# Kernel optimization log

Measured on AMD Instinct MI355X. Metric: run time of the kernel, lower is better.

Reference implementation:

```python
import math
import jax, jax.numpy as jnp
import numpy as np

# irreps: 128x0e + 64x1o + 32x2e  -> (mul, l, parity)
IRREPS = [(128, 0, 1), (64, 1, -1), (32, 2, 1)]
IR_SET = {(l, p) for _, l, p in IRREPS}
FEAT_DIM = sum(m * (2 * l + 1) for m, l, _ in IRREPS)   # 480
N_NODES = 32768
TOTAL_MUL = sum(m for m, _, _ in IRREPS)                # 224


def _su2_cg(j1, j2, j3, m1, m2, m3):
    if m1 + m2 != m3:
        return 0.0
    f = math.factorial
    pref = math.sqrt((2 * j3 + 1) * f(j3 + j1 - j2) * f(j3 - j1 + j2) * f(j1 + j2 - j3) / f(j1 + j2 + j3 + 1))
    pref *= math.sqrt(f(j3 + m3) * f(j3 - m3) * f(j1 - m1) * f(j1 + m1) * f(j2 - m2) * f(j2 + m2))
    s = 0.0
    vmin = max(0, j2 - j3 - m1, j1 - j3 + m2)
    vmax = min(j2 + m2, j1 - m1, j1 + j2 - j3)
    for v in range(vmin, vmax + 1):
        s += (-1.0) ** v / (f(v) * f(j1 + j2 - j3 - v) * f(j1 - m1 - v) * f(j2 + m2 - v) * f(j3 - j2 + m1 + v) * f(j3 - j1 - m2 + v))
    return pref * s


def _q(l):
    # change of basis real <- complex spherical harmonics (e3nn convention)
    q = np.zeros((2 * l + 1, 2 * l + 1), dtype=complex)
    for m in range(-l, 0):
        q[l + m, l + abs(m)] = 1 / np.sqrt(2)
        q[l + m, l - abs(m)] = -1j / np.sqrt(2)
    q[l, l] = 1.0
    for m in range(1, l + 1):
        q[l + m, l + abs(m)] = (-1) ** m / np.sqrt(2)
        q[l + m, l - abs(m)] = 1j * (-1) ** m / np.sqrt(2)
    return (-1j) ** l * q


def _wigner3j(l1, l2, l3):
    Cc = np.zeros((2 * l1 + 1, 2 * l2 + 1, 2 * l3 + 1))
    for m1 in range(-l1, l1 + 1):
        for m2 in range(-l2, l2 + 1):
            m3 = m1 + m2
            if -l3 <= m3 <= l3:
                Cc[l1 + m1, l2 + m2, l3 + m3] = _su2_cg(l1, l2, l3, m1, m2, m3)
    C = np.einsum('ai,bj,ck,abc->ijk', _q(l1), _q(l2), np.conj(_q(l3)), Cc.astype(complex))
    Cr, Ci = np.real(C), np.imag(C)
    C = Cr if np.linalg.norm(Cr) >= np.linalg.norm(Ci) else Ci
    return (C / np.linalg.norm(C)).astype(np.float32)


# CG-coupling paths ('uvu' connection, shared internal weights of shape [mul1, mul2])
PATHS = []
_off = 0
for _i1, (_m1, _l1, _p1) in enumerate(IRREPS):
    for _i2, (_m2, _l2, _p2) in enumerate(IRREPS):
        for _l3 in range(abs(_l1 - _l2), _l1 + _l2 + 1):
            _p3 = _p1 * _p2
            if (_l3, _p3) in IR_SET:
                PATHS.append((_i1, _i2, _l3, _p3, _off, _m1 * _m2))
                _off += _m1 * _m2
TPW_SIZE = _off  # 55296
W3J = {(IRREPS[i1][1], IRREPS[i2][1], l3): None for i1, i2, l3, _, _, _ in PATHS}
for (_l1, _l2, _l3) in list(W3J.keys()):
    W3J[(_l1, _l2, _l3)] = jnp.asarray(_wigner3j(_l1, _l2, _l3))
COUPLED_MUL = {}
for _i1, _i2, _l3, _p3, _, _ in PATHS:
    COUPLED_MUL[(_l3, _p3)] = COUPLED_MUL.get((_l3, _p3), 0) + IRREPS[_i1][0]


def _split(feat):
    blocks, o = [], 0
    for mul, l, _ in IRREPS:
        d = mul * (2 * l + 1)
        blocks.append(feat[:, o:o + d].reshape(feat.shape[0], mul, 2 * l + 1))
        o += d
    return blocks


def _merge(blocks):
    return jnp.concatenate([x.reshape(x.shape[0], -1) for x in blocks], axis=-1)


def _lin(blocks, ws):
    # e3nn o3.Linear between identical simplified irreps: per-l channel mixing, 1/sqrt(fan_in)
    return [jnp.einsum('nui,uv->nvi', x, w) / np.sqrt(x.shape[1]) for x, w in zip(blocks, ws)]


def _normgate(blocks, w1, b1, w2, b2):
    # invariants: raw scalars for l=0, channel norms for l>0
    invs = []
    for (mul, l, _), x in zip(IRREPS, blocks):
        invs.append(x[:, :, 0] if l == 0 else jnp.sqrt(jnp.sum(x * x, -1) + 1e-12))
    v = jnp.concatenate(invs, -1)                          # [N, TOTAL_MUL]
    vn = (v - v.mean(-1, keepdims=True)) / jnp.sqrt(v.var(-1, keepdims=True) + 1e-5)  # 'node' norm
    g = jax.nn.silu(jax.nn.silu(vn @ w1 + b1) @ w2 + b2)   # 2-layer MLP gate
    out, o = [], 0
    for (mul, l, _), x in zip(IRREPS, blocks):
        out.append(x * g[:, o:o + mul, None])
        o += mul
    return out


def _cg_couple(b1, b2, tp_w):
    grouped = {(0, 1): [], (1, -1): [], (2, 1): []}
    for i1, i2, l3, p3, off, size in PATHS:
        m1, l1, _ = IRREPS[i1]
        m2, l2, _ = IRREPS[i2]
        w = tp_w[off:off + size].reshape(m1, m2)
        t = jnp.einsum('nvj,uv->nuj', b2[i2], w) / np.sqrt(m2)   # mix v-channels into u (small intermediate)
        y = jnp.einsum('nui,nuj,ijk->nuk', b1[i1], t, W3J[(l1, l2, l3)])
        grouped[(l3, p3)].append(y)
    return {k: jnp.concatenate(v, axis=1) for k, v in grouped.items()}


def _forward(feat, pre_w0, pre_w1, pre_w2, pre_ng_w1, pre_ng_b1, pre_ng_w2, pre_ng_b2,
             tp_w, post_w0, post_w1, post_w2, post_ng_w1, post_ng_b1, post_ng_w2, post_ng_b2):
    blocks = _split(feat)
    pre = _normgate(_lin(blocks, (pre_w0, pre_w1, pre_w2)), pre_ng_w1, pre_ng_b1, pre_ng_w2, pre_ng_b2)
    coupled = _cg_couple(blocks, pre, tp_w)
    post_blocks = []
    for (mul, l, p), w in zip(IRREPS, (post_w0, post_w1, post_w2)):
        x = coupled[(l, p)]
        post_blocks.append(jnp.einsum('nui,uv->nvi', x, w) / np.sqrt(x.shape[1]))
    post = _normgate(post_blocks, post_ng_w1, post_ng_b1, post_ng_w2, post_ng_b2)
    # feat_dropout p=0.0 -> identity
    return feat + _merge(pre) + _merge(post)


def setup_inputs() -> dict:
    key = jax.random.key(0)
    ks = jax.random.split(key, 16)
    def n(k, shape):
        return jax.random.normal(k, shape, dtype=jnp.float32)
    return {
        'feat': n(ks[0], (N_NODES, FEAT_DIM)),
        'pre_w0': n(ks[1], (128, 128)),
        'pre_w1': n(ks[2], (64, 64)),
        'pre_w2': n(ks[3], (32, 32)),
        'pre_ng_w1': n(ks[4], (TOTAL_MUL, TOTAL_MUL)) / np.sqrt(TOTAL_MUL),
        'pre_ng_b1': jnp.zeros((TOTAL_MUL,), jnp.float32),
        'pre_ng_w2': n(ks[5], (TOTAL_MUL, TOTAL_MUL)) / np.sqrt(TOTAL_MUL),
        'pre_ng_b2': jnp.zeros((TOTAL_MUL,), jnp.float32),
        'tp_w': n(ks[6], (TPW_SIZE,)),
        'post_w0': n(ks[7], (COUPLED_MUL[(0, 1)], 128)),
        'post_w1': n(ks[8], (COUPLED_MUL[(1, -1)], 64)),
        'post_w2': n(ks[9], (COUPLED_MUL[(2, 1)], 32)),
        'post_ng_w1': n(ks[10], (TOTAL_MUL, TOTAL_MUL)) / np.sqrt(TOTAL_MUL),
        'post_ng_b1': jnp.zeros((TOTAL_MUL,), jnp.float32),
        'post_ng_w2': n(ks[11], (TOTAL_MUL, TOTAL_MUL)) / np.sqrt(TOTAL_MUL),
        'post_ng_b2': jnp.zeros((TOTAL_MUL,), jnp.float32),
    }


def reference(feat, pre_w0, pre_w1, pre_w2, pre_ng_w1, pre_ng_b1, pre_ng_w2, pre_ng_b2,
              tp_w, post_w0, post_w1, post_w2, post_ng_w1, post_ng_b1, post_ng_w2, post_ng_b2):
    return _forward(feat, pre_w0, pre_w1, pre_w2, pre_ng_w1, pre_ng_b1, pre_ng_w2, pre_ng_b2,
                    tp_w, post_w0, post_w1, post_w2, post_ng_w1, post_ng_b1, post_ng_w2, post_ng_b2)
```

## Files before the change

### kernel.cpp

```cpp
#include <hip/hip_runtime.h>
#include <cmath>
#include <complex>
#include <algorithm>

#define N_NODES  32768
#define FEAT_DIM 480
#define TMUL     224
#define NB       4
#define ST       3328

#define F0O 0
#define F1O 128
#define F2O 320
#define P0O 480
#define P1O 608
#define P2O 800
#define C0O 960
#define C1O 1184
#define C2O 2048
#define Q0O 960
#define Q1O 1088
#define Q2O 1280
#define INVO 1440
#define HO   1664
#define GO   1888

#define FSTR 240

typedef float f32x4 __attribute__((ext_vector_type(4)));
typedef short short8 __attribute__((ext_vector_type(8)));

__device__ __forceinline__ float siluf(float x){ return x * (1.0f/(1.0f + __expf(-x))); }
__device__ __forceinline__ f32x4 silu4(f32x4 x){
  f32x4 r; r.x=siluf(x.x); r.y=siluf(x.y); r.z=siluf(x.z); r.w=siluf(x.w); return r;
}
__device__ __forceinline__ f32x4 sqrt4(f32x4 x){
  f32x4 r; r.x=sqrtf(x.x); r.y=sqrtf(x.y); r.z=sqrtf(x.z); r.w=sqrtf(x.w); return r;
}

__device__ __forceinline__ float bfh(ushort h){ return __uint_as_float(((uint)h)<<16); }
__device__ __forceinline__ ushort f2bf(float f){
  uint u=__float_as_uint(f); return (ushort)((u + 0x7fffu + ((u>>16)&1u))>>16);
}
__device__ __forceinline__ f32x4 X0q(uint4 q){
  f32x4 r = {__uint_as_float(q.x<<16), __uint_as_float(q.x&0xffff0000u),
             __uint_as_float(q.y<<16), __uint_as_float(q.y&0xffff0000u)};
  return r;
}
__device__ __forceinline__ f32x4 X1q(uint4 q){
  f32x4 r = {__uint_as_float(q.z<<16), __uint_as_float(q.z&0xffff0000u),
             __uint_as_float(q.w<<16), __uint_as_float(q.w&0xffff0000u)};
  return r;
}
__device__ __forceinline__ f32x4 ldE(const uint* __restrict__ Lb, int e){
  uint2 q = *(const uint2*)&Lb[e*2];
  f32x4 r = {__uint_as_float(q.x<<16), __uint_as_float(q.x&0xffff0000u),
             __uint_as_float(q.y<<16), __uint_as_float(q.y&0xffff0000u)};
  return r;
}
__device__ __forceinline__ void stE(uint* __restrict__ Lb, int e, f32x4 x){
  uint2 q = { (uint)f2bf(x.x) | ((uint)f2bf(x.y)<<16),
              (uint)f2bf(x.z) | ((uint)f2bf(x.w)<<16) };
  *(uint2*)&Lb[e*2] = q;
}

struct W3Pack { float v[363]; };

static double factd(int n){ double f=1.0; for(int i=2;i<=n;++i) f*=(double)i; return f; }

static double su2_cg(int j1,int j2,int j3,int m1,int m2,int m3){
  if (m1+m2 != m3) return 0.0;
  double pref = std::sqrt((2.0*j3+1.0)*factd(j3+j1-j2)*factd(j3-j1+j2)*factd(j1+j2-j3)/factd(j1+j2+j3+1));
  pref *= std::sqrt(factd(j3+m3)*factd(j3-m3)*factd(j1-m1)*factd(j1+m1)*factd(j2-m2)*factd(j2+m2));
  double s=0.0;
  int vmin = std::max(0, std::max(j2-j3-m1, j1-j3+m2));
  int vmax = std::min(j2+m2, std::min(j1-m1, j1+j2-j3));
  for (int v=vmin; v<=vmax; ++v){
    double d = factd(v)*factd(j1+j2-j3-v)*factd(j1-m1-v)*factd(j2+m2-v)*factd(j3-j2+m1+v)*factd(j3-j1-m2+v);
    s += ((v&1)? -1.0 : 1.0)/d;
  }
  return pref*s;
}

typedef std::complex<double> cd;

static void qmat(int l, cd* q){
  int d=2*l+1;
  for (int a=0;a<d*d;++a) q[a]=cd(0,0);
  double is2 = 1.0/std::sqrt(2.0);
  for (int m=-l; m<0; ++m){
    int am=-m;
    q[(l+m)*d + (l+am)] = cd(is2,0);
    q[(l+m)*d + (l-am)] = cd(0,-is2);
  }
  q[l*d+l] = cd(1,0);
  for (int m=1;m<=l;++m){
    double sg = (m&1)? -1.0:1.0;
    q[(l+m)*d + (l+m)] = cd(sg*is2,0);
    q[(l+m)*d + (l-m)] = cd(0,sg*is2);
  }
  cd f = (l==0)? cd(1,0) : (l==1? cd(0,-1) : cd(-1,0));
  for (int a=0;a<d*d;++a) q[a]*=f;
}

static void wigner3j(int l1,int l2,int l3, float* out){
  int d1=2*l1+1,d2=2*l2+1,d3=2*l3+1;
  double Cc[5][5][5] = {};
  for (int m1=-l1;m1<=l1;++m1) for (int m2=-l2;m2<=l2;++m2){
    int m3=m1+m2;
    if (m3>=-l3 && m3<=l3) Cc[l1+m1][l2+m2][l3+m3] = su2_cg(l1,l2,l3,m1,m2,m3);
  }
  cd q1[25],q2[25],q3[25];
  qmat(l1,q1); qmat(l2,q2); qmat(l3,q3);
  double re[125], im[125];
  double nr=0, ni=0;
  for (int i=0;i<d1;++i) for (int j=0;j<d2;++j) for (int k=0;k<d3;++k){
    cd s(0,0);
    for (int a=0;a<d1;++a) for (int b=0;b<d2;++b) for (int c=0;c<d3;++c){
      double cc = Cc[a][b][c];
      if (cc != 0.0) s += q1[a*d1+i]*q2[b*d2+j]*std::conj(q3[c*d3+k])*cc;
    }
    int o=(i*d2+j)*d3+k;
    re[o]=s.real(); im[o]=s.imag();
    nr += s.real()*s.real(); ni += s.imag()*s.imag();
  }
  bool useRe = std::sqrt(nr) >= std::sqrt(ni);
  double nrm = std::sqrt(useRe? nr : ni);
  for (int o=0;o<d1*d2*d3;++o) out[o] = (float)((useRe? re[o] : im[o]) / nrm);
}

static W3Pack build_w3(){
  W3Pack W;
  wigner3j(0,0,0, W.v+0);
  wigner3j(0,1,1, W.v+1);
  wigner3j(0,2,2, W.v+10);
  wigner3j(1,0,1, W.v+35);
  wigner3j(1,1,0, W.v+44);
  wigner3j(1,1,2, W.v+53);
  wigner3j(1,2,1, W.v+98);
  wigner3j(2,0,2, W.v+143);
  wigner3j(2,1,1, W.v+168);
  wigner3j(2,2,0, W.v+213);
  wigner3j(2,2,2, W.v+238);
  return W;
}

__global__ __launch_bounds__(256) void prep_tpw(const float* __restrict__ tpw, float* __restrict__ wt)
{
  const int t = blockIdx.x*256 + threadIdx.x;
  if (t >= 55296) return;
  float v;
  if (t < 28672) {
    const int vv = t / 224, r = t - vv*224;
    int off, u;
    if (r < 128)      { off = 0;     u = r; }
    else if (r < 192) { off = 28672; u = r-128; }
    else              { off = 47104; u = r-192; }
    v = tpw[off + u*128 + vv] * 0.08838834764831845f;
  } else if (t < 47104) {
    const int t2 = t-28672; const int vv = t2/288, r = t2 - vv*288;
    int off, u;
    if (r < 128)      { off = 16384; u = r; }
    else if (r < 192) { off = 36864; u = r-128; }
    else if (r < 256) { off = 40960; u = r-192; }
    else              { off = 51200; u = r-256; }
    v = tpw[off + u*64 + vv] * 0.125f;
  } else {
    const int t3 = t-47104; const int vv = t3/256, r = t3 & 255;
    int off, u;
    if (r < 128)      { off = 24576; u = r; }
    else if (r < 192) { off = 45056; u = r-128; }
    else if (r < 224) { off = 53248; u = r-192; }
    else              { off = 54272; u = r-224; }
    v = tpw[off + u*32 + vv] * 0.17677669529663687f;
  }
  wt[t] = v;
}

__global__ __launch_bounds__(256) void prep_mlp(
  const float* __restrict__ pgw1, const float* __restrict__ pgw2,
  const float* __restrict__ qgw1, const float* __restrict__ qgw2,
  ushort* __restrict__ wb)
{
  const int t = blockIdx.x*256 + threadIdx.x;
  if (t >= 4*50176) return;
  const int mat = t / 50176, s = t - mat*50176;
  const float* src = (mat==0)? pgw1 : (mat==1)? pgw2 : (mat==2)? qgw1 : qgw2;
  const int e = s & 7, l = (s>>3) & 63, q = s >> 9;
  const int ct = q % 14, kt = q / 14;
  const int k = kt*32 + (l>>4)*8 + e;
  const int c = ct*16 + (l&15);
  wb[t] = f2bf(src[k*224 + c]);
}

template<int N>
__device__ __forceinline__ f32x4 matcolB(const float* __restrict__ Wg, const int wstride, const int col,
                                         const uint* __restrict__ Lb, const int inbase)
{
  f32x4 a0={}, a1={}, a2={}, a3={};
  const float* wp = Wg + col;
  #pragma unroll 2
  for (int u=0; u<N; u+=4) {
    const float wA = wp[(u+0)*wstride];
    const float wB = wp[(u+1)*wstride];
    const float wC = wp[(u+2)*wstride];
    const float wD = wp[(u+3)*wstride];
    const uint4 qa = *(const uint4*)&Lb[(inbase+u)*2];
    const uint4 qb = *(const uint4*)&Lb[(inbase+u+2)*2];
    a0 += X0q(qa)*wA;
    a1 += X1q(qa)*wB;
    a2 += X0q(qb)*wC;
    a3 += X1q(qb)*wD;
  }
  return (a0+a1)+(a2+a3);
}

template<int NJ, int M2, int JS>
__device__ __forceinline__ void tstageB(const float* __restrict__ wcol, const int wstride,
                                        const uint* __restrict__ Lb, const int pbase,
                                        f32x4 (&t)[NJ])
{
  f32x4 a0[NJ], a1[NJ];
  #pragma unroll
  for (int j=0;j<NJ;++j){ a0[j]=(f32x4){}; a1[j]=(f32x4){}; }
  #pragma unroll 2
  for (int v=0; v<M2; v+=2) {
    const float wA = wcol[v*wstride];
    const float wB = wcol[(v+1)*wstride];
    #pragma unroll
    for (int j=0;j<NJ;++j) {
      const uint4 q = *(const uint4*)&Lb[(pbase + j*JS + v)*2];
      a0[j] += X0q(q)*wA;
      a1[j] += X1q(q)*wB;
    }
  }
  #pragma unroll
  for (int j=0;j<NJ;++j) t[j] = a0[j]+a1[j];
}

__device__ __forceinline__ void normgateB(uint* __restrict__ Lb, ushort* __restrict__ Lb16,
                                          ushort* __restrict__ FT16, f32x4* __restrict__ sRed, const int c,
                                          const int B0, const int B1, const int B2,
                                          const ushort* __restrict__ wb1, const float* __restrict__ gb1,
                                          const ushort* __restrict__ wb2, const float* __restrict__ gb2)
{
  if (c < 128) {
    const uint2 q = *(const uint2*)&Lb[(B0+c)*2];
    *(uint2*)&Lb[(INVO+c)*2] = q;
  } else if (c < 192) {
    const int v = c-128;
    f32x4 s = {1e-12f,1e-12f,1e-12f,1e-12f};
    #pragma unroll
    for (int i=0;i<3;++i){ const f32x4 x = ldE(Lb, B1+i*64+v); s += x*x; }
    stE(Lb, INVO+c, sqrt4(s));
  } else if (c < 224) {
    const int v = c-192;
    f32x4 s = {1e-12f,1e-12f,1e-12f,1e-12f};
    #pragma unroll
    for (int i=0;i<5;++i){ const f32x4 x = ldE(Lb, B2+i*32+v); s += x*x; }
    stE(Lb, INVO+c, sqrt4(s));
  }
  __syncthreads();
  {
    const int w = c>>6, l = c&63;
    float s=0.f, s2=0.f, x;
    x = bfh(Lb16[(INVO+l)*4+w]);      s+=x; s2+=x*x;
    x = bfh(Lb16[(INVO+64+l)*4+w]);   s+=x; s2+=x*x;
    x = bfh(Lb16[(INVO+128+l)*4+w]);  s+=x; s2+=x*x;
    if (l < 32) { x = bfh(Lb16[(INVO+192+l)*4+w]); s+=x; s2+=x*x; }
    #pragma unroll
    for (int off=32; off>=1; off>>=1) {
      s  += __shfl_xor(s,  off, 64);
      s2 += __shfl_xor(s2, off, 64);
    }
    if (l==0) {
      const float m = s*(1.f/224.f);
      ((float*)&sRed[0])[w] = m;
      ((float*)&sRed[1])[w] = rsqrtf(s2*(1.f/224.f) - m*m + 1e-5f);
    }
  }
  __syncthreads();
  if (c < TMUL) {
    const f32x4 x = ldE(Lb, INVO+c);
    const f32x4 vn = (x - sRed[0])*sRed[1];
    FT16[0*FSTR+c]=f2bf(vn.x); FT16[1*FSTR+c]=f2bf(vn.y);
    FT16[2*FSTR+c]=f2bf(vn.z); FT16[3*FSTR+c]=f2bf(vn.w);
  }
  __syncthreads();

  const int wv = c>>6, ln = c&63;
  f32x4 m0={}, m1={}, m2={}, m3={};
  #pragma unroll
  for (int kt=0; kt<7; ++kt) {
    const short8 A = *(const short8*)&FT16[(ln&15)*FSTR + kt*32 + (ln>>4)*8];
    { const short8 B = *(const short8*)&wb1[((kt*14 + wv    )*64 + ln)*8];
      m0 = __builtin_amdgcn_mfma_f32_16x16x32_bf16(A, B, m0, 0, 0, 0); }
    { const short8 B = *(const short8*)&wb1[((kt*14 + wv + 4)*64 + ln)*8];
      m1 = __builtin_amdgcn_mfma_f32_16x16x32_bf16(A, B, m1, 0, 0, 0); }
    { const short8 B = *(const short8*)&wb1[((kt*14 + wv + 8)*64 + ln)*8];
      m2 = __builtin_amdgcn_mfma_f32_16x16x32_bf16(A, B, m2, 0, 0, 0); }
    if (wv < 2) {
      const short8 B = *(const short8*)&wb1[((kt*14 + wv +12)*64 + ln)*8];
      m3 = __builtin_amdgcn_mfma_f32_16x16x32_bf16(A, B, m3, 0, 0, 0);
    }
  }
  __syncthreads();
  if (ln < 16) {
    { const int ch=(wv   )*16+ln; const f32x4 h=silu4(m0+gb1[ch]);
      FT16[0*FSTR+ch]=f2bf(h.x); FT16[1*FSTR+ch]=f2bf(h.y); FT16[2*FSTR+ch]=f2bf(h.z); FT16[3*FSTR+ch]=f2bf(h.w); }
    { const int ch=(wv+4 )*16+ln; const f32x4 h=silu4(m1+gb1[ch]);
      FT16[0*FSTR+ch]=f2bf(h.x); FT16[1*FSTR+ch]=f2bf(h.y); FT16[2*FSTR+ch]=f2bf(h.z); FT16[3*FSTR+ch]=f2bf(h.w); }
    { const int ch=(wv+8 )*16+ln; const f32x4 h=silu4(m2+gb1[ch]);
      FT16[0*FSTR+ch]=f2bf(h.x); FT16[1*FSTR+ch]=f2bf(h.y); FT16[2*FSTR+ch]=f2bf(h.z); FT16[3*FSTR+ch]=f2bf(h.w); }
    if (wv < 2) {
      const int ch=(wv+12)*16+ln; const f32x4 h=silu4(m3+gb1[ch]);
      FT16[0*FSTR+ch]=f2bf(h.x); FT16[1*FSTR+ch]=f2bf(h.y); FT16[2*FSTR+ch]=f2bf(h.z); FT16[3*FSTR+ch]=f2bf(h.w); }
  }
  __syncthreads();
  f32x4 g0={}, g1={}, g2={}, g3={};
  #pragma unroll
  for (int kt=0; kt<7; ++kt) {
    const short8 A = *(const short8*)&FT16[(ln&15)*FSTR + kt*32 + (ln>>4)*8];
    { const short8 B = *(const short8*)&wb2[((kt*14 + wv    )*64 + ln)*8];
      g0 = __builtin_amdgcn_mfma_f32_16x16x32_bf16(A, B, g0, 0, 0, 0); }
    { const short8 B = *(const short8*)&wb2[((kt*14 + wv + 4)*64 + ln)*8];
      g1 = __builtin_amdgcn_mfma_f32_16x16x32_bf16(A, B, g1, 0, 0, 0); }
    { const short8 B = *(const short8*)&wb2[((kt*14 + wv + 8)*64 + ln)*8];
      g2 = __builtin_amdgcn_mfma_f32_16x16x32_bf16(A, B, g2, 0, 0, 0); }
    if (wv < 2) {
      const short8 B = *(const short8*)&wb2[((kt*14 + wv +12)*64 + ln)*8];
      g3 = __builtin_amdgcn_mfma_f32_16x16x32_bf16(A, B, g3, 0, 0, 0);
    }
  }
  if (ln < 16) {
    { const int ch=(wv   )*16+ln; stE(Lb, GO+ch, silu4(g0+gb2[ch])); }
    { const int ch=(wv+4 )*16+ln; stE(Lb, GO+ch, silu4(g1+gb2[ch])); }
    { const int ch=(wv+8 )*16+ln; stE(Lb, GO+ch, silu4(g2+gb2[ch])); }
    if (wv < 2) { const int ch=(wv+12)*16+ln; stE(Lb, GO+ch, silu4(g3+gb2[ch])); }
  }
  __syncthreads();
}

__device__ __forceinline__ void cg_rowB(const int r, const float* __restrict__ wt,
                                        const W3Pack& W, uint* __restrict__ Lb)
{
  f32x4 tb[3];
  tstageB<3,64,64>(wt + 28672 + r, 288, Lb, P1O, tb);
  if (r < 128) {
    const f32x4 f = ldE(Lb, F0O+r);
    #pragma unroll
    for (int k=0;k<3;++k) {
      f32x4 s = tb[0]*W.v[1+0*3+k] + tb[1]*W.v[1+1*3+k] + tb[2]*W.v[1+2*3+k];
      stE(Lb, C1O+k*288+r, f*s);
    }
  } else if (r < 192) {
    const int u=r-128;
    f32x4 y = {};
    #pragma unroll
    for (int i=0;i<3;++i) {
      f32x4 s = tb[0]*W.v[44+i*3+0] + tb[1]*W.v[44+i*3+1] + tb[2]*W.v[44+i*3+2];
      y += ldE(Lb, F1O+i*64+u)*s;
    }
    stE(Lb, C0O+128+u, y);
  } else if (r < 256) {
    const int u=r-192;
    f32x4 f[3];
    #pragma unroll
    for (int i=0;i<3;++i) f[i]=ldE(Lb, F1O+i*64+u);
    #pragma unroll
    for (int k=0;k<5;++k) {
      f32x4 y = {};
      #pragma unroll
      for (int i=0;i<3;++i) {
        f32x4 s = tb[0]*W.v[53+(i*3+0)*5+k] + tb[1]*W.v[53+(i*3+1)*5+k] + tb[2]*W.v[53+(i*3+2)*5+k];
        y += f[i]*s;
      }
      stE(Lb, C2O+k*256+128+u, y);
    }
  } else {
    const int u=r-256;
    f32x4 f[5];
    #pragma unroll
    for (int i=0;i<5;++i) f[i]=ldE(Lb, F2O+i*32+u);
    #pragma unroll
    for (int k=0;k<3;++k) {
      f32x4 y = {};
      #pragma unroll
      for (int i=0;i<5;++i) {
        f32x4 s = tb[0]*W.v[168+(i*3+0)*3+k] + tb[1]*W.v[168+(i*3+1)*3+k] + tb[2]*W.v[168+(i*3+2)*3+k];
        y += f[i]*s;
      }
      stE(Lb, C1O+k*288+256+u, y);
    }
  }
}

__device__ __forceinline__ void cg_rowC(const int r, const float* __restrict__ wt,
                                        const W3Pack& W, uint* __restrict__ Lb)
{
  f32x4 tc[5];
  tstageB<5,32,32>(wt + 47104 + r, 256, Lb, P2O, tc);
  if (r < 128) {
    const f32x4 f = ldE(Lb, F0O+r);
    #pragma unroll
    for (int k=0;k<5;++k) {
      f32x4 s = {};
      #pragma unroll
      for (int j=0;j<5;++j) s += tc[j]*W.v[10+j*5+k];
      stE(Lb, C2O+k*256+r, f*s);
    }
  } else if (r < 192) {
    const int u=r-128;
    f32x4 f[3];
    #pragma unroll
    for (int i=0;i<3;++i) f[i]=ldE(Lb, F1O+i*64+u);
    #pragma unroll
    for (int k=0;k<3;++k) {
      f32x4 y = {};
      #pragma unroll
      for (int i=0;i<3;++i) {
        f32x4 s = {};
        #pragma unroll
        for (int j=0;j<5;++j) s += tc[j]*W.v[98+(i*5+j)*3+k];
        y += f[i]*s;
      }
      stE(Lb, C1O+k*288+192+u, y);
    }
  } else if (r < 224) {
    const int u=r-192;
    f32x4 y = {};
    #pragma unroll
    for (int i=0;i<5;++i) {
      f32x4 s = {};
      #pragma unroll
      for (int j=0;j<5;++j) s += tc[j]*W.v[213+i*5+j];
      y += ldE(Lb, F2O+i*32+u)*s;
    }
    stE(Lb, C0O+192+u, y);
  } else {
    const int u=r-224;
    f32x4 f[5];
    #pragma unroll
    for (int i=0;i<5;++i) f[i]=ldE(Lb, F2O+i*32+u);
    #pragma unroll
    for (int k=0;k<5;++k) {
      f32x4 y = {};
      #pragma unroll
      for (int i=0;i<5;++i) {
        f32x4 s = {};
        #pragma unroll
        for (int j=0;j<5;++j) s += tc[j]*W.v[238+(i*5+j)*5+k];
        y += f[i]*s;
      }
      stE(Lb, C2O+k*256+224+u, y);
    }
  }
}

__global__ __launch_bounds__(256, 4) void fused4(
  const float* __restrict__ feat,
  const float* __restrict__ w0, const float* __restrict__ w1, const float* __restrict__ w2,
  const float* __restrict__ pgb1, const float* __restrict__ pgb2,
  const float* __restrict__ wt, const ushort* __restrict__ wb,
  const float* __restrict__ pw0, const float* __restrict__ pw1, const float* __restrict__ pw2,
  const float* __restrict__ qgb1, const float* __restrict__ qgb2,
  float* __restrict__ outp, const W3Pack W)
{
  __shared__ uint LbU[ST*2];
  __shared__ ushort FT16[16*FSTR];
  __shared__ f32x4 sRed[2];
  uint* Lb = LbU;
  ushort* Lb16 = (ushort*)LbU;
  const int c = threadIdx.x;
  const size_t gbase = (size_t)blockIdx.x * (FEAT_DIM*NB);

  {
    uint* FTz = (uint*)FT16;
    #pragma unroll
    for (int t=c; t<16*FSTR/2; t+=256) FTz[t] = 0;
  }

  for (int t=c; t<FEAT_DIM*NB; t+=256) {
    const float val = feat[gbase + t];
    const int nb = t / FEAT_DIM;
    const int ch = t - nb*FEAT_DIM;
    int loc;
    if (ch < 128) loc = F0O + ch;
    else if (ch < 320) { const int q = ch-128; const int u = q/3; loc = F1O + (q-u*3)*64 + u; }
    else               { const int q = ch-320; const int u = q/5; loc = F2O + (q-u*5)*32 + u; }
    Lb16[loc*4 + nb] = f2bf(val);
  }
  __syncthreads();

  {
    f32x4 a1, a2 = {};
    int o1, o2=-1; float s1, s2s=0.f;
    if (c < 128) { a1 = matcolB<128>(w0, 128, c, Lb, F0O); o1 = P0O+c; s1 = 0.08838834764831845f; }
    else { const int q=c-128; const int i=q>>6, v=q&63;
           a1 = matcolB<64>(w1, 64, v, Lb, F1O+i*64); o1 = P1O+i*64+v; s1 = 0.125f; }
    if (c < 64) { a2 = matcolB<64>(w1, 64, c, Lb, F1O+128); o2 = P1O+128+c; s2s = 0.125f; }
    else if (c < 224) { const int q=c-64; const int i=q>>5, v=q&31;
           a2 = matcolB<32>(w2, 32, v, Lb, F2O+i*32); o2 = P2O+i*32+v; s2s = 0.17677669529663687f; }
    stE(Lb, o1, a1*s1);
    if (o2 >= 0) stE(Lb, o2, a2*s2s);
  }
  __syncthreads();

  normgateB(Lb, Lb16, FT16, sRed, c, P0O, P1O, P2O, wb, pgb1, wb+50176, pgb2);
  if (c < 128) {
    stE(Lb, P0O+c, ldE(Lb,P0O+c)*ldE(Lb,GO+c));
  } else if (c < 192) {
    const int v=c-128; const f32x4 g=ldE(Lb,GO+c);
    #pragma unroll
    for (int i=0;i<3;++i) stE(Lb, P1O+i*64+v, ldE(Lb,P1O+i*64+v)*g);
  } else if (c < 224) {
    const int v=c-192; const f32x4 g=ldE(Lb,GO+c);
    #pragma unroll
    for (int i=0;i<5;++i) stE(Lb, P2O+i*32+v, ldE(Lb,P2O+i*32+v)*g);
  }
  __syncthreads();

  if (c < 224) {
    const f32x4 tA = matcolB<128>(wt, 224, c, Lb, P0O);
    if (c < 128) {
      stE(Lb, C0O+c, ldE(Lb,F0O+c)*tA*W.v[0]);
    } else if (c < 192) {
      const int u=c-128;
      const f32x4 f0=ldE(Lb,F1O+u), f1=ldE(Lb,F1O+64+u), f2=ldE(Lb,F1O+128+u);
      #pragma unroll
      for (int k=0;k<3;++k)
        stE(Lb, C1O+k*288+128+u, tA*(f0*W.v[35+k] + f1*W.v[38+k] + f2*W.v[41+k]));
    } else {
      const int u=c-192;
      f32x4 f[5];
      #pragma unroll
      for (int i=0;i<5;++i) f[i]=ldE(Lb,F2O+i*32+u);
      #pragma unroll
      for (int k=0;k<5;++k) {
        f32x4 y = {};
        #pragma unroll
        for (int i=0;i<5;++i) y += f[i]*W.v[143+i*5+k];
        stE(Lb, C2O+k*256+192+u, tA*y);
      }
    }
  }
  cg_rowB(c, wt, W, Lb);
  if (c >= 224) cg_rowB(c+32, wt, W, Lb);
  cg_rowC(c, wt, W, Lb);
  __syncthreads();

  {
    f32x4 pa, pb = {};
    int po1, po2=-1; float ps1, ps2=0.f;
    if (c < 128) { pa = matcolB<224>(pw0, 128, c, Lb, C0O); po1 = Q0O+c; ps1 = 0.06681531047810609f; }
    else { const int q=c-128; const int i=q>>6, v=q&63;
           pa = matcolB<288>(pw1, 64, v, Lb, C1O+i*288); po1 = Q1O+i*64+v; ps1 = 0.05892556509887896f; }
    if (c < 64) { pb = matcolB<288>(pw1, 64, c, Lb, C1O+2*288); po2 = Q1O+128+c; ps2 = 0.05892556509887896f; }
    else if (c < 224) { const int q=c-64; const int i=q>>5, v=q&31;
           pb = matcolB<256>(pw2, 32, v, Lb, C2O+i*256); po2 = Q2O+i*32+v; ps2 = 0.0625f; }
    __syncthreads();
    stE(Lb, po1, pa*ps1);
    if (po2 >= 0) stE(Lb, po2, pb*ps2);
  }
  __syncthreads();

  normgateB(Lb, Lb16, FT16, sRed, c, Q0O, Q1O, Q2O, wb+100352, qgb1, wb+150528, qgb2);

  for (int t=c; t<FEAT_DIM*NB; t+=256) {
    const int nb = t / FEAT_DIM;
    const int ch = t - nb*FEAT_DIM;
    float pre, q, g;
    if (ch < 128) {
      pre = bfh(Lb16[(P0O+ch)*4+nb]);
      q   = bfh(Lb16[(Q0O+ch)*4+nb]);
      g   = bfh(Lb16[(GO+ch)*4+nb]);
    } else if (ch < 320) {
      const int qq=ch-128; const int u=qq/3; const int o=(qq-u*3)*64+u;
      pre = bfh(Lb16[(P1O+o)*4+nb]);
      q   = bfh(Lb16[(Q1O+o)*4+nb]);
      g   = bfh(Lb16[(GO+128+u)*4+nb]);
    } else {
      const int qq=ch-320; const int u=qq/5; const int o=(qq-u*5)*32+u;
      pre = bfh(Lb16[(P2O+o)*4+nb]);
      q   = bfh(Lb16[(Q2O+o)*4+nb]);
      g   = bfh(Lb16[(GO+192+u)*4+nb]);
    }
    outp[gbase + t] = feat[gbase + t] + pre + q*g;
  }
}

extern "C" void kernel_launch(void* const* d_in, const int* in_sizes, int n_in,
                              void* d_out, int out_size, void* d_ws, size_t ws_size,
                              hipStream_t stream)
{
  (void)in_sizes; (void)n_in; (void)out_size; (void)ws_size;
  const float* feat  = (const float*)d_in[0];
  const float* prw0  = (const float*)d_in[1];
  const float* prw1  = (const float*)d_in[2];
  const float* prw2  = (const float*)d_in[3];
  const float* pngw1 = (const float*)d_in[4];
  const float* pngb1 = (const float*)d_in[5];
  const float* pngw2 = (const float*)d_in[6];
  const float* pngb2 = (const float*)d_in[7];
  const float* tpw   = (const float*)d_in[8];
  const float* pow0  = (const float*)d_in[9];
  const float* pow1  = (const float*)d_in[10];
  const float* pow2  = (const float*)d_in[11];
  const float* qngw1 = (const float*)d_in[12];
  const float* qngb1 = (const float*)d_in[13];
  const float* qngw2 = (const float*)d_in[14];
  const float* qngb2 = (const float*)d_in[15];

  float*  wt = (float*)d_ws;
  ushort* wb = (ushort*)((char*)d_ws + 55296*sizeof(float));

  W3Pack W = build_w3();

  prep_tpw<<<dim3(216), dim3(256), 0, stream>>>(tpw, wt);
  prep_mlp<<<dim3(784), dim3(256), 0, stream>>>(pngw1, pngw2, qngw1, qngw2, wb);

  fused4<<<dim3(N_NODES/NB), dim3(256), 0, stream>>>(
      feat, prw0, prw1, prw2, pngb1, pngb2,
      wt, wb, pow0, pow1, pow2, qngb1, qngb2,
      (float*)d_out, W);
}
```

Baseline: 921.4 us.

## Move pre/post equivariant linears to bf16 MFMA with prepacked weights

Adds a prep kernel that packs the pre- and post-linear weights into bf16 MFMA tile layout with the normalization scales folded in. Inside the fused kernel, both linears now run as 16x16x32 bf16 MFMA instead of scalar per-column FMA loops reading fp32 weights from global memory. Inputs and CG outputs are written into a new row-major bf16 shared buffer so they can be fed as MFMA A operands. This cuts scalar ALU work and global weight traffic, but raises shared-memory use and lowers the launch-bounds occupancy hint from 4 to 3 blocks, and MFMA tiles are only partly used for the small 4-node batch.

```diff
diff --git a/kernel.cpp b/kernel.cpp
--- a/kernel.cpp
+++ b/kernel.cpp
@@ -7,7 +7,6 @@
 #define FEAT_DIM 480
 #define TMUL     224
 #define NB       4
-#define ST       3328
 
 #define F0O 0
 #define F1O 128
@@ -15,15 +14,12 @@
 #define P0O 480
 #define P1O 608
 #define P2O 800
-#define C0O 960
-#define C1O 1184
-#define C2O 2048
 #define Q0O 960
 #define Q1O 1088
 #define Q2O 1280
 #define INVO 1440
-#define HO   1664
 #define GO   1888
+#define NMSZ 2112
 
 #define FSTR 240
 
@@ -62,6 +58,12 @@
   uint2 q = { (uint)f2bf(x.x) | ((uint)f2bf(x.y)<<16),
               (uint)f2bf(x.z) | ((uint)f2bf(x.w)<<16) };
   *(uint2*)&Lb[e*2] = q;
+}
+__device__ __forceinline__ void stF(ushort* __restrict__ p, int stride, int row0, int col, f32x4 y){
+  p[(row0+0)*stride+col]=f2bf(y.x);
+  p[(row0+1)*stride+col]=f2bf(y.y);
+  p[(row0+2)*stride+col]=f2bf(y.z);
+  p[(row0+3)*stride+col]=f2bf(y.w);
 }
 
 struct W3Pack { float v[363]; };
@@ -193,6 +195,27 @@
   wb[t] = f2bf(src[k*224 + c]);
 }
 
+__global__ __launch_bounds__(256) void prep_lin(
+  const float* __restrict__ w0, const float* __restrict__ w1, const float* __restrict__ w2,
+  const float* __restrict__ pw0, const float* __restrict__ pw1, const float* __restrict__ pw2,
+  ushort* __restrict__ wf)
+{
+  const int t = blockIdx.x*256 + threadIdx.x;
+  if (t >= 76800) return;
+  int s = t; const float* src; int ncols, nct; float sc;
+  if      (t < 16384) { src=w0;  ncols=128; nct=8; sc=0.08838834764831845f; }
+  else if (t < 20480) { s=t-16384; src=w1;  ncols=64;  nct=4; sc=0.125f; }
+  else if (t < 21504) { s=t-20480; src=w2;  ncols=32;  nct=2; sc=0.17677669529663687f; }
+  else if (t < 50176) { s=t-21504; src=pw0; ncols=128; nct=8; sc=0.06681531047810609f; }
+  else if (t < 68608) { s=t-50176; src=pw1; ncols=64;  nct=4; sc=0.05892556509887896f; }
+  else                { s=t-68608; src=pw2; ncols=32;  nct=2; sc=0.0625f; }
+  const int e = s & 7, l = (s>>3) & 63, tile = s >> 9;
+  const int ct = tile % nct, kt = tile / nct;
+  const int k = kt*32 + (l>>4)*8 + e;
+  const int c = ct*16 + (l&15);
+  wf[t] = f2bf(src[k*ncols + c] * sc);
+}
+
 template<int N>
 __device__ __forceinline__ f32x4 matcolB(const float* __restrict__ Wg, const int wstride, const int col,
                                          const uint* __restrict__ Lb, const int inbase)
@@ -342,7 +365,9 @@
 }
 
 __device__ __forceinline__ void cg_rowB(const int r, const float* __restrict__ wt,
-                                        const W3Pack& W, uint* __restrict__ Lb)
+                                        const W3Pack& W, uint* __restrict__ Lb,
+                                        ushort* __restrict__ C0f, ushort* __restrict__ C1f,
+                                        ushort* __restrict__ C2f)
 {
   f32x4 tb[3];
   tstageB<3,64,64>(wt + 28672 + r, 288, Lb, P1O, tb);
@@ -351,7 +376,7 @@
     #pragma unroll
     for (int k=0;k<3;++k) {
       f32x4 s = tb[0]*W.v[1+0*3+k] + tb[1]*W.v[1+1*3+k] + tb[2]*W.v[1+2*3+k];
-      stE(Lb, C1O+k*288+r, f*s);
+      stF(C1f, 288, k*4, r, f*s);
     }
   } else if (r < 192) {
     const int u=r-128;
@@ -361,7 +386,7 @@
       f32x4 s = tb[0]*W.v[44+i*3+0] + tb[1]*W.v[44+i*3+1] + tb[2]*W.v[44+i*3+2];
       y += ldE(Lb, F1O+i*64+u)*s;
     }
-    stE(Lb, C0O+128+u, y);
+    stF(C0f, 224, 0, 128+u, y);
   } else if (r < 256) {
     const int u=r-192;
     f32x4 f[3];
@@ -375,7 +400,7 @@
         f32x4 s = tb[0]*W.v[53+(i*3+0)*5+k] + tb[1]*W.v[53+(i*3+1)*5+k] + tb[2]*W.v[53+(i*3+2)*5+k];
         y += f[i]*s;
       }
-      stE(Lb, C2O+k*256+128+u, y);
+      stF(C2f, 256, k*4, 128+u, y);
     }
   } else {
     const int u=r-256;
@@ -390,13 +415,15 @@
         f32x4 s = tb[0]*W.v[168+(i*3+0)*3+k] + tb[1]*W.v[168+(i*3+1)*3+k] + tb[2]*W.v[168+(i*3+2)*3+k];
         y += f[i]*s;
       }
-      stE(Lb, C1O+k*288+256+u, y);
+      stF(C1f, 288, k*4, 256+u, y);
     }
   }
 }
 
 __device__ __forceinline__ void cg_rowC(const int r, const float* __restrict__ wt,
-                                        const W3Pack& W, uint* __restrict__ Lb)
+                                        const W3Pack& W, uint* __restrict__ Lb,
+                                        ushort* __restrict__ C0f, ushort* __restrict__ C1f,
+                                        ushort* __restrict__ C2f)
 {
   f32x4 tc[5];
   tstageB<5,32,32>(wt + 47104 + r, 256, Lb, P2O, tc);
@@ -407,7 +434,7 @@
       f32x4 s = {};
       #pragma unroll
       for (int j=0;j<5;++j) s += tc[j]*W.v[10+j*5+k];
-      stE(Lb, C2O+k*256+r, f*s);
+      stF(C2f, 256, k*4, r, f*s);
     }
   } else if (r < 192) {
     const int u=r-128;
@@ -424,7 +451,7 @@
         for (int j=0;j<5;++j) s += tc[j]*W.v[98+(i*5+j)*3+k];
         y += f[i]*s;
       }
-      stE(Lb, C1O+k*288+192+u, y);
+      stF(C1f, 288, k*4, 192+u, y);
     }
   } else if (r < 224) {
     const int u=r-192;
@@ -436,7 +463,7 @@
       for (int j=0;j<5;++j) s += tc[j]*W.v[213+i*5+j];
       y += ldE(Lb, F2O+i*32+u)*s;
     }
-    stE(Lb, C0O+192+u, y);
+    stF(C0f, 224, 0, 192+u, y);
   } else {
     const int u=r-224;
     f32x4 f[5];
@@ -452,57 +479,87 @@
         for (int j=0;j<5;++j) s += tc[j]*W.v[238+(i*5+j)*5+k];
         y += f[i]*s;
       }
-      stE(Lb, C2O+k*256+224+u, y);
-    }
-  }
-}
-
-__global__ __launch_bounds__(256, 4) void fused4(
+      stF(C2f, 256, k*4, 224+u, y);
+    }
+  }
+}
+
+__global__ __launch_bounds__(256, 3) void fused4(
   const float* __restrict__ feat,
-  const float* __restrict__ w0, const float* __restrict__ w1, const float* __restrict__ w2,
   const float* __restrict__ pgb1, const float* __restrict__ pgb2,
-  const float* __restrict__ wt, const ushort* __restrict__ wb,
-  const float* __restrict__ pw0, const float* __restrict__ pw1, const float* __restrict__ pw2,
+  const float* __restrict__ wt, const ushort* __restrict__ wb, const ushort* __restrict__ wf,
   const float* __restrict__ qgb1, const float* __restrict__ qgb2,
   float* __restrict__ outp, const W3Pack W)
 {
-  __shared__ uint LbU[ST*2];
-  __shared__ ushort FT16[16*FSTR];
+  __shared__ uint LbU[NMSZ*2];
+  __shared__ ushort BF[16384];
   __shared__ f32x4 sRed[2];
   uint* Lb = LbU;
   ushort* Lb16 = (ushort*)LbU;
+  ushort* C0f = BF;
+  ushort* C1f = BF + 3584;
+  ushort* C2f = BF + 8192;
+  ushort* FT16 = BF;
+  ushort* F0f = BF + 8192;
+  ushort* F1f = BF + 10240;
+  ushort* F2f = BF + 11264;
   const int c = threadIdx.x;
+  const int wv = c>>6, ln = c&63;
   const size_t gbase = (size_t)blockIdx.x * (FEAT_DIM*NB);
-
-  {
-    uint* FTz = (uint*)FT16;
-    #pragma unroll
-    for (int t=c; t<16*FSTR/2; t+=256) FTz[t] = 0;
-  }
 
   for (int t=c; t<FEAT_DIM*NB; t+=256) {
     const float val = feat[gbase + t];
     const int nb = t / FEAT_DIM;
     const int ch = t - nb*FEAT_DIM;
-    int loc;
-    if (ch < 128) loc = F0O + ch;
-    else if (ch < 320) { const int q = ch-128; const int u = q/3; loc = F1O + (q-u*3)*64 + u; }
-    else               { const int q = ch-320; const int u = q/5; loc = F2O + (q-u*5)*32 + u; }
-    Lb16[loc*4 + nb] = f2bf(val);
+    const ushort b = f2bf(val);
+    if (ch < 128) {
+      Lb16[(F0O+ch)*4 + nb] = b;
+      F0f[nb*128 + ch] = b;
+    } else if (ch < 320) {
+      const int q = ch-128; const int u = q/3; const int i = q-u*3;
+      Lb16[(F1O + i*64 + u)*4 + nb] = b;
+      F1f[(i*4+nb)*64 + u] = b;
+    } else {
+      const int q = ch-320; const int u = q/5; const int i = q-u*5;
+      Lb16[(F2O + i*32 + u)*4 + nb] = b;
+      if (i < 4) F2f[(i*4+nb)*32 + u] = b;
+      else       F2f[(16+nb)*32 + u] = b;
+    }
   }
   __syncthreads();
 
   {
-    f32x4 a1, a2 = {};
-    int o1, o2=-1; float s1, s2s=0.f;
-    if (c < 128) { a1 = matcolB<128>(w0, 128, c, Lb, F0O); o1 = P0O+c; s1 = 0.08838834764831845f; }
-    else { const int q=c-128; const int i=q>>6, v=q&63;
-           a1 = matcolB<64>(w1, 64, v, Lb, F1O+i*64); o1 = P1O+i*64+v; s1 = 0.125f; }
-    if (c < 64) { a2 = matcolB<64>(w1, 64, c, Lb, F1O+128); o2 = P1O+128+c; s2s = 0.125f; }
-    else if (c < 224) { const int q=c-64; const int i=q>>5, v=q&31;
-           a2 = matcolB<32>(w2, 32, v, Lb, F2O+i*32); o2 = P2O+i*32+v; s2s = 0.17677669529663687f; }
-    stE(Lb, o1, a1*s1);
-    if (o2 >= 0) stE(Lb, o2, a2*s2s);
+    #pragma unroll
+    for (int half=0; half<2; ++half) {
+      const int ct = wv*2+half;
+      f32x4 acc = {};
+      #pragma unroll
+      for (int kt=0; kt<4; ++kt) {
+        const short8 A = *(const short8*)&F0f[(ln&15)*128 + kt*32 + (ln>>4)*8];
+        const short8 B = *(const short8*)&wf[((kt*8+ct)*64+ln)*8];
+        acc = __builtin_amdgcn_mfma_f32_16x16x32_bf16(A,B,acc,0,0,0);
+      }
+      if (ln < 16) stE(Lb, P0O + ct*16 + ln, acc);
+    }
+    {
+      f32x4 acc = {};
+      #pragma unroll
+      for (int kt=0; kt<2; ++kt) {
+        const short8 A = *(const short8*)&F1f[(ln&15)*64 + kt*32 + (ln>>4)*8];
+        const short8 B = *(const short8*)&wf[16384 + ((kt*4+wv)*64+ln)*8];
+        acc = __builtin_amdgcn_mfma_f32_16x16x32_bf16(A,B,acc,0,0,0);
+      }
+      if (ln < 48) stE(Lb, P1O + (ln>>4)*64 + wv*16 + (ln&15), acc);
+    }
+    {
+      const int tile = wv>>1, ct = wv&1;
+      const short8 A = *(const short8*)&F2f[(tile*16+(ln&15))*32 + (ln>>4)*8];
+      const short8 B = *(const short8*)&wf[20480 + (ct*64+ln)*8];
+      f32x4 acc = {};
+      acc = __builtin_amdgcn_mfma_f32_16x16x32_bf16(A,B,acc,0,0,0);
+      if (tile==0) stE(Lb, P2O + (ln>>4)*32 + ct*16 + (ln&15), acc);
+      else if (ln < 16) stE(Lb, P2O + 128 + ct*16 + ln, acc);
+    }
   }
   __syncthreads();
 
@@ -523,13 +580,13 @@
   if (c < 224) {
     const f32x4 tA = matcolB<128>(wt, 224, c, Lb, P0O);
     if (c < 128) {
-      stE(Lb, C0O+c, ldE(Lb,F0O+c)*tA*W.v[0]);
+      stF(C0f, 224, 0, c, ldE(Lb,F0O+c)*tA*W.v[0]);
     } else if (c < 192) {
       const int u=c-128;
       const f32x4 f0=ldE(Lb,F1O+u), f1=ldE(Lb,F1O+64+u), f2=ldE(Lb,F1O+128+u);
       #pragma unroll
       for (int k=0;k<3;++k)
-        stE(Lb, C1O+k*288+128+u, tA*(f0*W.v[35+k] + f1*W.v[38+k] + f2*W.v[41+k]));
+        stF(C1f, 288, k*4, 128+u, tA*(f0*W.v[35+k] + f1*W.v[38+k] + f2*W.v[41+k]));
     } else {
       const int u=c-192;
       f32x4 f[5];
@@ -540,27 +597,50 @@
         f32x4 y = {};
         #pragma unroll
         for (int i=0;i<5;++i) y += f[i]*W.v[143+i*5+k];
-        stE(Lb, C2O+k*256+192+u, tA*y);
-      }
-    }
-  }
-  cg_rowB(c, wt, W, Lb);
-  if (c >= 224) cg_rowB(c+32, wt, W, Lb);
-  cg_rowC(c, wt, W, Lb);
+        stF(C2f, 256, k*4, 192+u, tA*y);
+      }
+    }
+  }
+  cg_rowB(c, wt, W, Lb, C0f, C1f, C2f);
+  if (c >= 224) cg_rowB(c+32, wt, W, Lb, C0f, C1f, C2f);
+  cg_rowC(c, wt, W, Lb, C0f, C1f, C2f);
   __syncthreads();
 
   {
-    f32x4 pa, pb = {};
-    int po1, po2=-1; float ps1, ps2=0.f;
-    if (c < 128) { pa = matcolB<224>(pw0, 128, c, Lb, C0O); po1 = Q0O+c; ps1 = 0.06681531047810609f; }
-    else { const int q=c-128; const int i=q>>6, v=q&63;
-           pa = matcolB<288>(pw1, 64, v, Lb, C1O+i*288); po1 = Q1O+i*64+v; ps1 = 0.05892556509887896f; }
-    if (c < 64) { pb = matcolB<288>(pw1, 64, c, Lb, C1O+2*288); po2 = Q1O+128+c; ps2 = 0.05892556509887896f; }
-    else if (c < 224) { const int q=c-64; const int i=q>>5, v=q&31;
-           pb = matcolB<256>(pw2, 32, v, Lb, C2O+i*256); po2 = Q2O+i*32+v; ps2 = 0.0625f; }
-    __syncthreads();
-    stE(Lb, po1, pa*ps1);
-    if (po2 >= 0) stE(Lb, po2, pb*ps2);
+    #pragma unroll
+    for (int half=0; half<2; ++half) {
+      const int ct = wv*2+half;
+      f32x4 acc = {};
+      #pragma unroll
+      for (int kt=0; kt<7; ++kt) {
+        const short8 A = *(const short8*)&C0f[(ln&15)*224 + kt*32 + (ln>>4)*8];
+        const short8 B = *(const short8*)&wf[21504 + ((kt*8+ct)*64+ln)*8];
+        acc = __builtin_amdgcn_mfma_f32_16x16x32_bf16(A,B,acc,0,0,0);
+      }
+      if (ln < 16) stE(Lb, Q0O + ct*16 + ln, acc);
+    }
+    {
+      f32x4 acc = {};
+      #pragma unroll
+      for (int kt=0; kt<9; ++kt) {
+        const short8 A = *(const short8*)&C1f[(ln&15)*288 + kt*32 + (ln>>4)*8];
+        const short8 B = *(const short8*)&wf[50176 + ((kt*4+wv)*64+ln)*8];
+        acc = __builtin_amdgcn_mfma_f32_16x16x32_bf16(A,B,acc,0,0,0);
+      }
+      if (ln < 48) stE(Lb, Q1O + (ln>>4)*64 + wv*16 + (ln&15), acc);
+    }
+    {
+      const int tile = wv>>1, ct = wv&1;
+      f32x4 acc = {};
+      #pragma unroll
+      for (int kt=0; kt<8; ++kt) {
+        const short8 A = *(const short8*)&C2f[(tile*16+(ln&15))*256 + kt*32 + (ln>>4)*8];
+        const short8 B = *(const short8*)&wf[68608 + ((kt*2+ct)*64+ln)*8];
+        acc = __builtin_amdgcn_mfma_f32_16x16x32_bf16(A,B,acc,0,0,0);
+      }
+      if (tile==0) stE(Lb, Q2O + (ln>>4)*32 + ct*16 + (ln&15), acc);
+      else if (ln < 16) stE(Lb, Q2O + 128 + ct*16 + ln, acc);
+    }
   }
   __syncthreads();
 
@@ -612,15 +692,16 @@
   const float* qngb2 = (const float*)d_in[15];
 
   float*  wt = (float*)d_ws;
-  ushort* wb = (ushort*)((char*)d_ws + 55296*sizeof(float));
+  ushort* wb = (ushort*)((char*)d_ws + 221184);
+  ushort* wf = (ushort*)((char*)d_ws + 221184 + 401408);
 
   W3Pack W = build_w3();
 
   prep_tpw<<<dim3(216), dim3(256), 0, stream>>>(tpw, wt);
   prep_mlp<<<dim3(784), dim3(256), 0, stream>>>(pngw1, pngw2, qngw1, qngw2, wb);
+  prep_lin<<<dim3(300), dim3(256), 0, stream>>>(prw0, prw1, prw2, pow0, pow1, pow2, wf);
 
   fused4<<<dim3(N_NODES/NB), dim3(256), 0, stream>>>(
-      feat, prw0, prw1, prw2, pngb1, pngb2,
-      wt, wb, pow0, pow1, pow2, qngb1, qngb2,
+      feat, pngb1, pngb2, wt, wb, wf, qngb1, qngb2,
       (float*)d_out, W);
 }
```

Result: faster. 836.0 us (-9.3%).
